# Kernel optimization log

Hardware: AMD Instinct MI355X
Metric: run time of the kernel (lower is better)

Reference implementation:

```python
import jax, jax.numpy as jnp
import numpy as np

MIN_V, MAX_V, NORM = 0.0, 4.0, 4.0
NUM_HEADS = 8
BN_EPS = 1e-5

@jax.custom_vjp
def quant(x):
    return jnp.round(jnp.clip(x, MIN_V, MAX_V))

def _quant_fwd(x):
    return jnp.round(jnp.clip(x, MIN_V, MAX_V)), x

def _quant_bwd(x, g):
    # straight-through: zero grad outside [min, max]
    return (jnp.where((x < MIN_V) | (x > MAX_V), 0.0, g),)

quant.defvjp(_quant_fwd, _quant_bwd)

def spike(x):
    return quant(x) / NORM

def conv_bn(x, w, gamma, beta, mean, var):
    # 1x1 conv (no bias) + BatchNorm2d (eval mode, running stats)
    y = jnp.einsum('oc,bchw->bohw', w, x)
    s = gamma / jnp.sqrt(var + BN_EPS)
    return y * s[None, :, None, None] + (beta - mean * s)[None, :, None, None]


def setup_inputs() -> dict:
    key = jax.random.key(0)
    B, C, H, W = 8, 384, 64, 64
    ks = jax.random.split(key, 21)
    d = {'x': jax.random.normal(ks[0], (B, C, H, W), jnp.float32)}
    i = 1
    for p in ('q', 'k', 'v', 'p'):
        d[f'{p}_w'] = jax.random.normal(ks[i], (C, C), jnp.float32) * 0.05; i += 1
        d[f'{p}_gamma'] = jax.random.uniform(ks[i], (C,), jnp.float32, 0.5, 1.5); i += 1
        d[f'{p}_beta'] = jax.random.normal(ks[i], (C,), jnp.float32) * 0.1; i += 1
        d[f'{p}_mean'] = jax.random.normal(ks[i], (C,), jnp.float32) * 0.1; i += 1
        d[f'{p}_var'] = jax.random.uniform(ks[i], (C,), jnp.float32, 0.5, 1.5); i += 1
    return d


def reference(x, q_w, q_gamma, q_beta, q_mean, q_var,
              k_w, k_gamma, k_beta, k_mean, k_var,
              v_w, v_gamma, v_beta, v_mean, v_var,
              p_w, p_gamma, p_beta, p_mean, p_var):
    B, C, H, W = x.shape
    N = H * W
    hd = C // NUM_HEADS
    scale = hd ** -0.5

    xs = spike(x)
    q = spike(conv_bn(xs, q_w, q_gamma, q_beta, q_mean, q_var))
    k = spike(conv_bn(xs, k_w, k_gamma, k_beta, k_mean, k_var))
    v = spike(conv_bn(xs, v_w, v_gamma, v_beta, v_mean, v_var))

    # (B,C,H,W) -> (B,heads,N,hd); channel c = h*hd + d
    def to_heads(t):
        return t.reshape(B, NUM_HEADS, hd, N).transpose(0, 1, 3, 2)

    q, k, v = to_heads(q), to_heads(k), to_heads(v)

    # softmax-free attention: (q @ k^T) @ v == q @ (k^T @ v)  -> O(N*d^2)
    kv = jnp.einsum('bhnd,bhne->bhde', k, v)          # [B,H,hd,hd]
    attn = jnp.einsum('bhnd,bhde->bhne', q, kv) * (scale * 2)  # [B,H,N,hd]

    # back to (B, C_v, N): torch does transpose(2,3).reshape(B,C_v,N)
    a = attn.transpose(0, 1, 3, 2).reshape(B, C, N)
    a = spike(a).reshape(B, C, H, W)
    out = conv_bn(a, p_w, p_gamma, p_beta, p_mean, p_var)
    return out
```

## Files before the change

### kernel.cpp

```cpp
#include <hip/hip_runtime.h>
#include <stdint.h>

#define B_  8
#define C_  384
#define N_  4096
#define NH_ 8
#define HD_ 48
#define CB_ (C_*N_)
#define KS2 768

typedef __attribute__((ext_vector_type(8))) short short8;
typedef __attribute__((ext_vector_type(8))) _Float16 half8;
typedef __attribute__((ext_vector_type(4))) float f32x4;

struct P5 { const float *w, *g, *be, *mu, *va; };
struct W4 { const float *w0, *w1, *w2, *w3; };

__device__ __forceinline__ float b2f(unsigned short u) {
    union { unsigned int i; float f; } c; c.i = ((unsigned int)u) << 16; return c.f;
}
__device__ __forceinline__ unsigned short f2b(float f) {
    union { float f; unsigned int i; } c; c.f = f;
    return (unsigned short)((c.i + 0x7FFFu + ((c.i >> 16) & 1u)) >> 16);
}
__device__ __forceinline__ unsigned short f2h(float f) {
    union { _Float16 h; unsigned short u; } c; c.h = (_Float16)f; return c.u;
}
__device__ __forceinline__ float spikef(float f) {
    f = fminf(fmaxf(f, 0.0f), 4.0f);
    return rintf(f) * 0.25f;
}
__device__ __forceinline__ void async16(const void* g, void* l) {
    __builtin_amdgcn_global_load_lds((const __attribute__((address_space(1))) void*)g,
                                     (__attribute__((address_space(3))) void*)l, 16, 0, 0);
}

__global__ __launch_bounds__(256) void k_prep(W4 ws4, unsigned short* __restrict__ wsp,
                                              float* __restrict__ kvf) {
    int idx = blockIdx.x * 256 + threadIdx.x;
    if (idx >= 589824) return;
    if (idx < 147456) kvf[idx] = 0.0f;
    int mat = idx / 147456, rem = idx % 147456;
    int o = rem / 384, c = rem % 384;
    const float* W = (mat == 0) ? ws4.w0 : (mat == 1) ? ws4.w1 : (mat == 2) ? ws4.w2 : ws4.w3;
    float w = W[o * 384 + c];
    _Float16 hh = (fabsf(w) < 6.103515625e-05f) ? (_Float16)0 : (_Float16)w;
    float r1 = w - (float)hh;
    float s  = r1 * 4096.0f;
    union { _Float16 h; unsigned short u; } ch, cl;
    ch.h = hh; cl.h = (_Float16)s;
    unsigned short* row = wsp + (size_t)mat * 384 * KS2 + (size_t)o * KS2 + c;
    row[0] = cl.u; row[384] = ch.u;
}

__global__ __launch_bounds__(256) void k0_spike_T(const float* __restrict__ x,
                                                  unsigned short* __restrict__ xst) {
    int nt = blockIdx.x, ct = blockIdx.y, b = blockIdx.z;
    int t = threadIdx.x;
    __shared__ __attribute__((aligned(16))) unsigned short sm[64][68];
    int n0 = nt * 64, c0 = ct * 64;
    const float* xb = x + (size_t)b * CB_;
    #pragma unroll
    for (int i = 0; i < 4; ++i) {
        int c = (t >> 4) + 16 * i;
        int seg = t & 15;
        float4 d = *(const float4*)(xb + (size_t)(c0 + c) * N_ + n0 + seg * 4);
        unsigned short v[4];
        v[0] = f2h(spikef(d.x)); v[1] = f2h(spikef(d.y));
        v[2] = f2h(spikef(d.z)); v[3] = f2h(spikef(d.w));
        *(uint2*)&sm[c][seg * 4] = *(const uint2*)v;
    }
    __syncthreads();
    unsigned short* ob = xst + (size_t)b * CB_;
    #pragma unroll
    for (int i = 0; i < 2; ++i) {
        int flat = i * 256 + t;
        int n = flat >> 3, segc = flat & 7;
        unsigned short v[8];
        #pragma unroll
        for (int j = 0; j < 8; ++j) v[j] = sm[segc * 8 + j][n];
        *(uint4*)(ob + (size_t)(n0 + n) * C_ + c0 + segc * 8) = *(const uint4*)v;
    }
}

__global__ __launch_bounds__(256) void k1_qkv(const unsigned short* __restrict__ xst,
                                              const unsigned short* __restrict__ wsp,
                                              P5 pq, P5 pk, P5 pv,
                                              unsigned short* __restrict__ qs,
                                              unsigned short* __restrict__ ks,
                                              unsigned short* __restrict__ vs) {
    int gid = blockIdx.x;
    int xcd = gid & 7, idx = gid >> 3;
    int pairSlot = idx / 9, mt = idx - pairSlot * 9;
    int p = xcd * 32 + pairSlot;
    int ntile = p >> 3, b = p & 7;
    int mat = mt / 3;
    int orow0 = (mt % 3) * 128;
    int n0 = ntile * 128;
    int t = threadIdx.x, lane = t & 63, wvv = t >> 6;
    int wr = wvv >> 1, wc = wvv & 1;

    __shared__ __attribute__((aligned(16))) short lds[17408];
    P5 pp = (mat == 0) ? pq : (mat == 1 ? pk : pv);
    const unsigned short* abase = xst + (size_t)b * CB_;
    const unsigned short* wbase = wsp + (size_t)mat * 384 * KS2;

    f32x4 acc[4][4] = {};
    for (int kk = 0; kk < KS2; kk += 64) {
        if (kk == 384) {
            #pragma unroll
            for (int mi = 0; mi < 4; ++mi)
                #pragma unroll
                for (int ni = 0; ni < 4; ++ni)
                    acc[mi][ni] = acc[mi][ni] * 0.000244140625f;
        }
        int ck = (kk >= 384) ? kk - 384 : kk;
        #pragma unroll
        for (int j = 0; j < 4; ++j) {
            int row = wvv * 32 + j * 8 + (lane >> 3);
            int g = (lane & 7) ^ (row & 7);
            async16(abase + (size_t)(n0 + row) * C_ + ck + g * 8, lds + (wvv * 32 + j * 8) * 64);
        }
        #pragma unroll
        for (int j = 0; j < 4; ++j) {
            int row = wvv * 32 + j * 8 + (lane >> 3);
            int g = (lane & 7) ^ (row & 7);
            async16(wbase + (size_t)(orow0 + row) * KS2 + kk + g * 8, lds + 8192 + (wvv * 32 + j * 8) * 64);
        }
        __syncthreads();
        #pragma unroll
        for (int ksb = 0; ksb < 2; ++ksb) {
            half8 af[4], bfr[4];
            #pragma unroll
            for (int mi = 0; mi < 4; ++mi) {
                int row = wr * 64 + mi * 16 + (lane & 15);
                int s = (ksb * 4 + (lane >> 4)) ^ (row & 7);
                af[mi] = *(const half8*)&lds[row * 64 + s * 8];
            }
            #pragma unroll
            for (int ni = 0; ni < 4; ++ni) {
                int row = wc * 64 + ni * 16 + (lane & 15);
                int s = (ksb * 4 + (lane >> 4)) ^ (row & 7);
                bfr[ni] = *(const half8*)&lds[8192 + row * 64 + s * 8];
            }
            #pragma unroll
            for (int mi = 0; mi < 4; ++mi)
                #pragma unroll
                for (int ni = 0; ni < 4; ++ni)
                    acc[mi][ni] = __builtin_amdgcn_mfma_f32_16x16x32_f16(af[mi], bfr[ni], acc[mi][ni], 0, 0, 0);
        }
        __syncthreads();
    }

    float s_bn[4], t_bn[4];
    #pragma unroll
    for (int ni = 0; ni < 4; ++ni) {
        int o = orow0 + wc * 64 + ni * 16 + (lane & 15);
        float g = pp.g[o], be = pp.be[o], mu = pp.mu[o], va = pp.va[o];
        float s = g / sqrtf(va + 1e-5f);
        s_bn[ni] = s; t_bn[ni] = be - mu * s;
    }
    unsigned short* esm = (unsigned short*)lds;

    if (mat != 0) {
        #pragma unroll
        for (int mi = 0; mi < 4; ++mi)
            #pragma unroll
            for (int ni = 0; ni < 4; ++ni) {
                int ol = wc * 64 + ni * 16 + (lane & 15);
                int nb = wr * 64 + mi * 16 + (lane >> 4) * 4;
                unsigned short vv[4];
                #pragma unroll
                for (int r = 0; r < 4; ++r)
                    vv[r] = f2b(spikef(acc[mi][ni][r] * s_bn[ni] + t_bn[ni]));
                *(uint2*)&esm[ol * 136 + nb] = *(const uint2*)vv;
            }
        __syncthreads();
        unsigned short* dst = ((mat == 1) ? ks : vs) + (size_t)b * CB_;
        #pragma unroll
        for (int i = 0; i < 8; ++i) {
            int o = (t >> 4) + 16 * i;
            int seg = t & 15;
            uint4 d = *(const uint4*)&esm[o * 136 + seg * 8];
            *(uint4*)(dst + (size_t)(orow0 + o) * N_ + n0 + seg * 8) = d;
        }
    } else {
        #pragma unroll
        for (int mi = 0; mi < 4; ++mi)
            #pragma unroll
            for (int ni = 0; ni < 4; ++ni) {
                int ol = wc * 64 + ni * 16 + (lane & 15);
                int nb = wr * 64 + mi * 16 + (lane >> 4) * 4;
                #pragma unroll
                for (int r = 0; r < 4; ++r)
                    esm[(nb + r) * 136 + ol] = f2b(spikef(acc[mi][ni][r] * s_bn[ni] + t_bn[ni]));
            }
        __syncthreads();
        #pragma unroll
        for (int i = 0; i < 8; ++i) {
            int n = (t >> 4) + 16 * i;
            int seg = t & 15;
            uint4 d = *(const uint4*)&esm[n * 136 + seg * 8];
            *(uint4*)(qs + ((size_t)b * N_ + n0 + n) * C_ + orow0 + seg * 8) = d;
        }
    }
}

__global__ __launch_bounds__(256) void k2_kv(const unsigned short* __restrict__ ks,
                                             const unsigned short* __restrict__ vs,
                                             float* __restrict__ kvf) {
    int id = blockIdx.x;
    int b = id >> 7, h = (id >> 4) & 7, ck = id & 15;
    int t = threadIdx.x, lane = t & 63, w = t >> 6;
    const unsigned short* kb = ks + (size_t)b * CB_ + h * HD_ * N_;
    const unsigned short* vb = vs + (size_t)b * CB_ + h * HD_ * N_;
    int kbase = ck * 256 + w * 64;

    f32x4 acc[3][3] = {};
    #pragma unroll
    for (int kk = 0; kk < 64; kk += 32) {
        int n = kbase + kk + (lane >> 4) * 8;
        short8 af[3], bfr[3];
        #pragma unroll
        for (int di = 0; di < 3; ++di)
            af[di] = *(const short8*)(kb + (size_t)((lane & 15) + 16 * di) * N_ + n);
        #pragma unroll
        for (int ei = 0; ei < 3; ++ei)
            bfr[ei] = *(const short8*)(vb + (size_t)((lane & 15) + 16 * ei) * N_ + n);
        #pragma unroll
        for (int di = 0; di < 3; ++di)
            #pragma unroll
            for (int ei = 0; ei < 3; ++ei)
                acc[di][ei] = __builtin_amdgcn_mfma_f32_16x16x32_bf16(af[di], bfr[ei], acc[di][ei], 0, 0, 0);
    }
    __shared__ float red[4][48][48];
    #pragma unroll
    for (int di = 0; di < 3; ++di)
        #pragma unroll
        for (int ei = 0; ei < 3; ++ei) {
            int d0 = di * 16 + (lane >> 4) * 4;
            int e = ei * 16 + (lane & 15);
            #pragma unroll
            for (int r = 0; r < 4; ++r) red[w][d0 + r][e] = acc[di][ei][r];
        }
    __syncthreads();
    for (int i = t; i < 2304; i += 256) {
        int e = i / 48, d = i % 48;
        float sum = red[0][d][e] + red[1][d][e] + red[2][d][e] + red[3][d][e];
        atomicAdd(&kvf[(b * NH_ + h) * 2304 + e * 48 + d], sum);
    }
}

__global__ __launch_bounds__(256) void k3_attn(const unsigned short* __restrict__ qs,
                                               const float* __restrict__ kvf,
                                               unsigned short* __restrict__ as_) {
    int id = blockIdx.x;
    int hg = id & 1, nt = (id >> 1) & 63, b = id >> 7;
    int t = threadIdx.x, lane = t & 63, w = t >> 6;
    int nb0 = nt * 64;
    __shared__ __attribute__((aligned(16))) unsigned short ldsq[64 * 24 * 8];
    __shared__ __attribute__((aligned(16))) unsigned short ldsh[48 * 72];
    __shared__ __attribute__((aligned(16))) unsigned short ldsl[48 * 72];

    const unsigned short* qb = qs + ((size_t)b * N_ + nb0) * C_ + hg * 192;
    #pragma unroll
    for (int i = 0; i < 6; ++i) {
        int g = (i * 4 + w) * 64;
        int f = g + lane;
        int row = f / 24, sc = f % 24;
        int c = sc ^ (row & 7);
        async16(qb + (size_t)row * C_ + c * 8, ldsq + (size_t)g * 8);
    }
    const float* kvb = kvf + ((size_t)(b * NH_ + hg * 4)) * 2304;
    const float S2 = 0.28867513459481287f;
    int quad = lane >> 4;
    int qrow = w * 16 + (lane & 15);

    for (int hl = 0; hl < 4; ++hl) {
        __syncthreads();
        const float* kvh = kvb + hl * 2304;
        for (int i = t; i < 48 * 64; i += 256) {
            int e = i >> 6, d = i & 63;
            unsigned short h16 = 0, l16 = 0;
            if (d < 48) {
                float v = kvh[e * 48 + d];
                h16 = f2b(v);
                l16 = f2b(v - b2f(h16));
            }
            ldsh[e * 72 + d] = h16;
            ldsl[e * 72 + d] = l16;
        }
        __syncthreads();

        f32x4 acc[3] = {};
        #pragma unroll
        for (int ksb = 0; ksb < 2; ++ksb) {
            int c = hl * 6 + ksb * 4 + quad;
            int cc = c > 23 ? 23 : c;
            int slot = cc ^ (qrow & 7);
            short8 a = *(const short8*)&ldsq[(qrow * 24 + slot) * 8];
            #pragma unroll
            for (int ei = 0; ei < 3; ++ei) {
                int e = ei * 16 + (lane & 15);
                short8 bh = *(const short8*)&ldsh[e * 72 + ksb * 32 + quad * 8];
                short8 bl = *(const short8*)&ldsl[e * 72 + ksb * 32 + quad * 8];
                acc[ei] = __builtin_amdgcn_mfma_f32_16x16x32_bf16(a, bh, acc[ei], 0, 0, 0);
                acc[ei] = __builtin_amdgcn_mfma_f32_16x16x32_bf16(a, bl, acc[ei], 0, 0, 0);
            }
        }
        #pragma unroll
        for (int ei = 0; ei < 3; ++ei) {
            int col = hl * 48 + ei * 16 + (lane & 15);
            int ch = col >> 3, j = col & 7;
            #pragma unroll
            for (int r = 0; r < 4; ++r) {
                int row = w * 16 + quad * 4 + r;
                ldsq[(row * 24 + (ch ^ (row & 7))) * 8 + j] = f2h(spikef(acc[ei][r] * S2));
            }
        }
    }
    __syncthreads();
    unsigned short* ob = as_ + ((size_t)b * N_ + nb0) * C_ + hg * 192;
    #pragma unroll
    for (int i = 0; i < 6; ++i) {
        int f = i * 256 + t;
        int row = f / 24, sc = f % 24;
        int slot = sc ^ (row & 7);
        uint4 d = *(const uint4*)&ldsq[(row * 24 + slot) * 8];
        *(uint4*)(ob + (size_t)row * C_ + sc * 8) = d;
    }
}

__global__ __launch_bounds__(256) void k4_pconv(const unsigned short* __restrict__ as_,
                                                const unsigned short* __restrict__ wsp,
                                                P5 pp,
                                                float* __restrict__ out) {
    int gid = blockIdx.x;
    int xcd = gid & 7, idx = gid >> 3;
    int pairSlot = idx / 3, mt = idx - pairSlot * 3;
    int p = xcd * 32 + pairSlot;
    int ntile = p >> 3, b = p & 7;
    int orow0 = mt * 128;
    int n0 = ntile * 128;
    int t = threadIdx.x, lane = t & 63, wvv = t >> 6;
    int wr = wvv >> 1, wc = wvv & 1;

    __shared__ __attribute__((aligned(16))) char ldsb[33792];
    short* lds = (short*)ldsb;
    const unsigned short* abase = as_ + (size_t)b * CB_;
    const unsigned short* wbase = wsp + (size_t)3 * 384 * KS2;

    f32x4 acc[4][4] = {};
    for (int kk = 0; kk < KS2; kk += 64) {
        if (kk == 384) {
            #pragma unroll
            for (int mi = 0; mi < 4; ++mi)
                #pragma unroll
                for (int ni = 0; ni < 4; ++ni)
                    acc[mi][ni] = acc[mi][ni] * 0.000244140625f;
        }
        int ck = (kk >= 384) ? kk - 384 : kk;
        #pragma unroll
        for (int j = 0; j < 4; ++j) {
            int row = wvv * 32 + j * 8 + (lane >> 3);
            int g = (lane & 7) ^ (row & 7);
            async16(abase + (size_t)(n0 + row) * C_ + ck + g * 8, lds + (wvv * 32 + j * 8) * 64);
        }
        #pragma unroll
        for (int j = 0; j < 4; ++j) {
            int row = wvv * 32 + j * 8 + (lane >> 3);
            int g = (lane & 7) ^ (row & 7);
            async16(wbase + (size_t)(orow0 + row) * KS2 + kk + g * 8, lds + 8192 + (wvv * 32 + j * 8) * 64);
        }
        __syncthreads();
        #pragma unroll
        for (int ksb = 0; ksb < 2; ++ksb) {
            half8 af[4], bfr[4];
            #pragma unroll
            for (int mi = 0; mi < 4; ++mi) {
                int row = wr * 64 + mi * 16 + (lane & 15);
                int s = (ksb * 4 + (lane >> 4)) ^ (row & 7);
                af[mi] = *(const half8*)&lds[row * 64 + s * 8];
            }
            #pragma unroll
            for (int ni = 0; ni < 4; ++ni) {
                int row = wc * 64 + ni * 16 + (lane & 15);
                int s = (ksb * 4 + (lane >> 4)) ^ (row & 7);
                bfr[ni] = *(const half8*)&lds[8192 + row * 64 + s * 8];
            }
            #pragma unroll
            for (int mi = 0; mi < 4; ++mi)
                #pragma unroll
                for (int ni = 0; ni < 4; ++ni)
                    acc[mi][ni] = __builtin_amdgcn_mfma_f32_16x16x32_f16(af[mi], bfr[ni], acc[mi][ni], 0, 0, 0);
        }
        __syncthreads();
    }

    float s_bn[4], t_bn[4];
    #pragma unroll
    for (int ni = 0; ni < 4; ++ni) {
        int o = orow0 + wc * 64 + ni * 16 + (lane & 15);
        float g = pp.g[o], be = pp.be[o], mu = pp.mu[o], va = pp.va[o];
        float s = g / sqrtf(va + 1e-5f);
        s_bn[ni] = s; t_bn[ni] = be - mu * s;
    }
    float* fsm = (float*)ldsb;
    for (int half = 0; half < 2; ++half) {
        __syncthreads();
        if (wc == half) {
            #pragma unroll
            for (int mi = 0; mi < 4; ++mi)
                #pragma unroll
                for (int ni = 0; ni < 4; ++ni) {
                    int ol = ni * 16 + (lane & 15);
                    int nl = wr * 64 + mi * 16 + (lane >> 4) * 4;
                    f32x4 vv;
                    #pragma unroll
                    for (int r = 0; r < 4; ++r)
                        vv[r] = acc[mi][ni][r] * s_bn[ni] + t_bn[ni];
                    *(f32x4*)&fsm[ol * 132 + nl] = vv;
                }
        }
        __syncthreads();
        #pragma unroll
        for (int i = 0; i < 8; ++i) {
            int f = i * 256 + t;
            int o = f >> 5, slot = f & 31;
            f32x4 vv = *(const f32x4*)&fsm[o * 132 + slot * 4];
            *(f32x4*)(out + ((size_t)b * C_ + orow0 + half * 64 + o) * N_ + n0 + slot * 4) = vv;
        }
    }
}

extern "C" void kernel_launch(void* const* d_in, const int* in_sizes, int n_in,
                              void* d_out, int out_size, void* d_ws, size_t ws_size,
                              hipStream_t stream) {
    P5 pq { (const float*)d_in[1],  (const float*)d_in[2],  (const float*)d_in[3],
            (const float*)d_in[4],  (const float*)d_in[5] };
    P5 pk { (const float*)d_in[6],  (const float*)d_in[7],  (const float*)d_in[8],
            (const float*)d_in[9],  (const float*)d_in[10] };
    P5 pv { (const float*)d_in[11], (const float*)d_in[12], (const float*)d_in[13],
            (const float*)d_in[14], (const float*)d_in[15] };
    P5 pp { (const float*)d_in[16], (const float*)d_in[17], (const float*)d_in[18],
            (const float*)d_in[19], (const float*)d_in[20] };
    W4 w4 { pq.w, pk.w, pv.w, pp.w };

    char* ws = (char*)d_ws;
    const size_t S = (size_t)B_ * C_ * N_ * 2;
    unsigned short* xst = (unsigned short*)ws;
    unsigned short* qs  = (unsigned short*)(ws + S);
    unsigned short* ks  = (unsigned short*)(ws + 2 * S + 256);
    unsigned short* vs  = (unsigned short*)(ws + 3 * S + 512);
    float*          kvf = (float*)(ws + 4 * S + 768);
    unsigned short* wsp = (unsigned short*)(ws + 4 * S + 768 + 589824);
    unsigned short* as_ = xst;

    k_prep<<<2304, 256, 0, stream>>>(w4, wsp, kvf);
    k0_spike_T<<<dim3(64, 6, 8), 256, 0, stream>>>((const float*)d_in[0], xst);
    k1_qkv<<<2304, 256, 0, stream>>>(xst, wsp, pq, pk, pv, qs, ks, vs);
    k2_kv<<<1024, 256, 0, stream>>>(ks, vs, kvf);
    k3_attn<<<1024, 256, 0, stream>>>(qs, kvf, as_);
    k4_pconv<<<768, 256, 0, stream>>>(as_, wsp, pp, (float*)d_out);
}
```

Before: 268.4 us.

## Fuse prep kernels and compute K^T V per head without split-K atomics

```diff
diff --git a/kernel.cpp b/kernel.cpp
--- a/kernel.cpp
+++ b/kernel.cpp
@@ -35,51 +35,51 @@
                                      (__attribute__((address_space(3))) void*)l, 16, 0, 0);
 }
 
-__global__ __launch_bounds__(256) void k_prep(W4 ws4, unsigned short* __restrict__ wsp,
-                                              float* __restrict__ kvf) {
-    int idx = blockIdx.x * 256 + threadIdx.x;
-    if (idx >= 589824) return;
-    if (idx < 147456) kvf[idx] = 0.0f;
-    int mat = idx / 147456, rem = idx % 147456;
-    int o = rem / 384, c = rem % 384;
-    const float* W = (mat == 0) ? ws4.w0 : (mat == 1) ? ws4.w1 : (mat == 2) ? ws4.w2 : ws4.w3;
-    float w = W[o * 384 + c];
-    _Float16 hh = (fabsf(w) < 6.103515625e-05f) ? (_Float16)0 : (_Float16)w;
-    float r1 = w - (float)hh;
-    float s  = r1 * 4096.0f;
-    union { _Float16 h; unsigned short u; } ch, cl;
-    ch.h = hh; cl.h = (_Float16)s;
-    unsigned short* row = wsp + (size_t)mat * 384 * KS2 + (size_t)o * KS2 + c;
-    row[0] = cl.u; row[384] = ch.u;
-}
-
-__global__ __launch_bounds__(256) void k0_spike_T(const float* __restrict__ x,
-                                                  unsigned short* __restrict__ xst) {
-    int nt = blockIdx.x, ct = blockIdx.y, b = blockIdx.z;
+__global__ __launch_bounds__(256) void kprep0(const float* __restrict__ x,
+                                              unsigned short* __restrict__ xst,
+                                              W4 ws4, unsigned short* __restrict__ wsp) {
+    int bid = blockIdx.x;
     int t = threadIdx.x;
     __shared__ __attribute__((aligned(16))) unsigned short sm[64][68];
-    int n0 = nt * 64, c0 = ct * 64;
-    const float* xb = x + (size_t)b * CB_;
-    #pragma unroll
-    for (int i = 0; i < 4; ++i) {
-        int c = (t >> 4) + 16 * i;
-        int seg = t & 15;
-        float4 d = *(const float4*)(xb + (size_t)(c0 + c) * N_ + n0 + seg * 4);
-        unsigned short v[4];
-        v[0] = f2h(spikef(d.x)); v[1] = f2h(spikef(d.y));
-        v[2] = f2h(spikef(d.z)); v[3] = f2h(spikef(d.w));
-        *(uint2*)&sm[c][seg * 4] = *(const uint2*)v;
-    }
-    __syncthreads();
-    unsigned short* ob = xst + (size_t)b * CB_;
-    #pragma unroll
-    for (int i = 0; i < 2; ++i) {
-        int flat = i * 256 + t;
-        int n = flat >> 3, segc = flat & 7;
-        unsigned short v[8];
-        #pragma unroll
-        for (int j = 0; j < 8; ++j) v[j] = sm[segc * 8 + j][n];
-        *(uint4*)(ob + (size_t)(n0 + n) * C_ + c0 + segc * 8) = *(const uint4*)v;
+    if (bid < 3072) {
+        int nt = bid & 63, rest = bid >> 6;
+        int ct = rest % 6, b = rest / 6;
+        int n0 = nt * 64, c0 = ct * 64;
+        const float* xb = x + (size_t)b * CB_;
+        #pragma unroll
+        for (int i = 0; i < 4; ++i) {
+            int c = (t >> 4) + 16 * i;
+            int seg = t & 15;
+            float4 d = *(const float4*)(xb + (size_t)(c0 + c) * N_ + n0 + seg * 4);
+            unsigned short v[4];
+            v[0] = f2h(spikef(d.x)); v[1] = f2h(spikef(d.y));
+            v[2] = f2h(spikef(d.z)); v[3] = f2h(spikef(d.w));
+            *(uint2*)&sm[c][seg * 4] = *(const uint2*)v;
+        }
+        __syncthreads();
+        unsigned short* ob = xst + (size_t)b * CB_;
+        #pragma unroll
+        for (int i = 0; i < 2; ++i) {
+            int flat = i * 256 + t;
+            int n = flat >> 3, segc = flat & 7;
+            unsigned short v[8];
+            #pragma unroll
+            for (int j = 0; j < 8; ++j) v[j] = sm[segc * 8 + j][n];
+            *(uint4*)(ob + (size_t)(n0 + n) * C_ + c0 + segc * 8) = *(const uint4*)v;
+        }
+    } else {
+        int idx = (bid - 3072) * 256 + t;
+        int mat = idx / 147456, rem = idx % 147456;
+        int o = rem / 384, c = rem % 384;
+        const float* W = (mat == 0) ? ws4.w0 : (mat == 1) ? ws4.w1 : (mat == 2) ? ws4.w2 : ws4.w3;
+        float w = W[o * 384 + c];
+        _Float16 hh = (fabsf(w) < 6.103515625e-05f) ? (_Float16)0 : (_Float16)w;
+        float r1 = w - (float)hh;
+        float s  = r1 * 4096.0f;
+        union { _Float16 h; unsigned short u; } ch, cl;
+        ch.h = hh; cl.h = (_Float16)s;
+        unsigned short* row = wsp + (size_t)mat * 384 * KS2 + (size_t)o * KS2 + c;
+        row[0] = cl.u; row[384] = ch.u;
     }
 }
 
@@ -210,16 +210,14 @@
                                              const unsigned short* __restrict__ vs,
                                              float* __restrict__ kvf) {
     int id = blockIdx.x;
-    int b = id >> 7, h = (id >> 4) & 7, ck = id & 15;
+    int b = id >> 3, h = id & 7;
     int t = threadIdx.x, lane = t & 63, w = t >> 6;
     const unsigned short* kb = ks + (size_t)b * CB_ + h * HD_ * N_;
     const unsigned short* vb = vs + (size_t)b * CB_ + h * HD_ * N_;
-    int kbase = ck * 256 + w * 64;
 
     f32x4 acc[3][3] = {};
-    #pragma unroll
-    for (int kk = 0; kk < 64; kk += 32) {
-        int n = kbase + kk + (lane >> 4) * 8;
+    for (int kk = 0; kk < 1024; kk += 32) {
+        int n = w * 1024 + kk + (lane >> 4) * 8;
         short8 af[3], bfr[3];
         #pragma unroll
         for (int di = 0; di < 3; ++di)
@@ -244,10 +242,10 @@
             for (int r = 0; r < 4; ++r) red[w][d0 + r][e] = acc[di][ei][r];
         }
     __syncthreads();
+    float* dst = kvf + (size_t)(b * NH_ + h) * 2304;
     for (int i = t; i < 2304; i += 256) {
         int e = i / 48, d = i % 48;
-        float sum = red[0][d][e] + red[1][d][e] + red[2][d][e] + red[3][d][e];
-        atomicAdd(&kvf[(b * NH_ + h) * 2304 + e * 48 + d], sum);
+        dst[e * 48 + d] = red[0][d][e] + red[1][d][e] + red[2][d][e] + red[3][d][e];
     }
 }
 
@@ -456,10 +454,9 @@
     unsigned short* wsp = (unsigned short*)(ws + 4 * S + 768 + 589824);
     unsigned short* as_ = xst;
 
-    k_prep<<<2304, 256, 0, stream>>>(w4, wsp, kvf);
-    k0_spike_T<<<dim3(64, 6, 8), 256, 0, stream>>>((const float*)d_in[0], xst);
+    kprep0<<<5376, 256, 0, stream>>>((const float*)d_in[0], xst, w4, wsp);
     k1_qkv<<<2304, 256, 0, stream>>>(xst, wsp, pq, pk, pv, qs, ks, vs);
-    k2_kv<<<1024, 256, 0, stream>>>(ks, vs, kvf);
+    k2_kv<<<64, 256, 0, stream>>>(ks, vs, kvf);
     k3_attn<<<1024, 256, 0, stream>>>(qs, kvf, as_);
     k4_pconv<<<768, 256, 0, stream>>>(as_, wsp, pp, (float*)d_out);
 }
```

After: 268.8 us. About the same (+0.1%).
